# Kernel tuning notes

Measured on AMD Instinct MI355X. Metric: run time of the kernel, lower is better.

The kernel has to match this reference:

```python
import jax, jax.numpy as jnp
import numpy as np

EPS = 1e-5


def setup_inputs() -> dict:
    key = jax.random.key(0)
    k1, k2, k3 = jax.random.split(key, 3)
    B, D, T = 16, 256, 4096
    K = 2048
    x = jax.random.normal(k1, (B, D, T), dtype=jnp.float32)
    embedding_sum = jax.random.normal(k2, (K, D), dtype=jnp.float32)
    cluster_usage = jax.random.uniform(k3, (K,), dtype=jnp.float32)
    return {"x": x, "embedding_sum": embedding_sum, "cluster_usage": cluster_usage}


def reference(x, embedding_sum, cluster_usage):
    # embedding property: embedding_sum / clamp(cluster_usage, min=eps)
    emb = embedding_sum / jnp.clip(cluster_usage, EPS, None)[:, None]  # [K, D]
    B, D, T = x.shape
    x_flat = jnp.transpose(x, (0, 2, 1)).reshape(B * T, D)  # (b t) d
    # compute faithfully (clamped for numerical safety).
    x2 = jnp.sum(x_flat * x_flat, axis=-1, keepdims=True)      # [BT, 1]
    e2 = jnp.sum(emb * emb, axis=-1)                           # [K]
    d2 = x2 - 2.0 * (x_flat @ emb.T) + e2[None, :]             # [BT, K]
    distances = jnp.sqrt(jnp.clip(d2, 0.0, None))
    codes = jnp.argmin(distances, axis=-1).reshape(B, 1, T)    # int codes
    # decode: embedding gather, b t d -> b d t
    decoded = jnp.transpose(emb[codes[:, 0, :]], (0, 2, 1))    # [B, D, T]
    return codes, decoded
```

## Files before the change

kernel.cpp:

```cpp
#include <hip/hip_runtime.h>
#include <hip/hip_fp16.h>
#include <cmath>

#define EPS 1e-5f
#define TAU 0.15f
#define RP  8

#define Bn 16
#define Dn 256
#define Tn 4096
#define Kn 2048

typedef unsigned short ushort_t;
typedef __attribute__((ext_vector_type(8))) _Float16 f16x8;
typedef __attribute__((ext_vector_type(4))) float f32x4;

__device__ __forceinline__ unsigned short f2h(float v) {
    return __half_as_ushort(__float2half_rn(v));
}

#define GLOAD_LDS16(gp, lp) __builtin_amdgcn_global_load_lds( \
    (const __attribute__((address_space(1))) unsigned int*)(gp), \
    (__attribute__((address_space(3))) unsigned int*)(lp), 16, 0, 0)

__global__ __launch_bounds__(256) void prep_kernel(
    const float* __restrict__ es, const float* __restrict__ usage,
    float* __restrict__ emb, ushort_t* __restrict__ e16,
    float* __restrict__ bias, float4* __restrict__ embT4,
    int* __restrict__ counter)
{
    __shared__ float sh[256];
    __shared__ float wsum[4];
    const int k = blockIdx.x;
    const int d = threadIdx.x;
    const float inv = 1.0f / fmaxf(usage[k], EPS);
    const float v = es[(size_t)k * Dn + d] * inv;
    emb[(size_t)k * Dn + d] = v;
    e16[(size_t)k * Dn + d] = f2h(fminf(fmaxf(v, -65504.f), 65504.f));
    sh[d] = v;
    float sq = v * v;
    #pragma unroll
    for (int off = 32; off > 0; off >>= 1) sq += __shfl_down(sq, off, 64);
    const int lane = d & 63, wv = d >> 6;
    if (lane == 0) wsum[wv] = sq;
    __syncthreads();
    if (d < 64)
        embT4[(size_t)d * Kn + k] = make_float4(sh[4*d], sh[4*d+1], sh[4*d+2], sh[4*d+3]);
    if (d == 0) {
        bias[k] = 0.5f * (wsum[0] + wsum[1] + wsum[2] + wsum[3]);
        if (k == 0) *counter = 0;
    }
}

#define BARRIER_PIN()                                                         \
    __builtin_amdgcn_s_barrier();                                             \
    __builtin_amdgcn_sched_barrier(0)

#define STAGE_B(dst, kcc, hh)                                                 \
    {                                                                         \
        _Pragma("unroll")                                                     \
        for (int r = 0; r < 4; ++r) {                                         \
            const int c   = r * 512 + tid;                                    \
            const int row = c >> 4;                                           \
            const int col = (((c & 15) ^ (row & 15)) << 3);                   \
            GLOAD_LDS16(e16 + ((size_t)((kcc) * 128 + row)) * Dn + (hh) * 128 + col, \
                        (dst) + ((r * 512 + (wid << 6)) << 3));               \
        }                                                                     \
    }

#define COMPUTE_ACC(bbuf, afArr)                                              \
    {                                                                         \
        __builtin_amdgcn_s_setprio(1);                                        \
        _Pragma("unroll")                                                     \
        for (int ks = 0; ks < 4; ++ks)                                        \
            _Pragma("unroll")                                                 \
            for (int j = 0; j < 8; ++j) {                                     \
                const f16x8 bf = *(const f16x8*)(                             \
                    &(bbuf)[((j << 4) + l15) * 128 +                          \
                            ((((ks << 2) | quad) ^ l15) << 3)]);              \
                _Pragma("unroll")                                             \
                for (int i = 0; i < 2; ++i)                                   \
                    acc[i][j] = __builtin_amdgcn_mfma_f32_16x16x32_f16(       \
                        afArr[ks * 2 + i], bf, acc[i][j], 0, 0, 0);           \
            }                                                                 \
        __builtin_amdgcn_s_setprio(0);                                        \
    }

__global__ __launch_bounds__(512, 2) void gemm_argmax(
    const float* __restrict__ x, const ushort_t* __restrict__ e16,
    const float* __restrict__ bias_g, int* __restrict__ codes_i,
    float* __restrict__ codes_f, int* __restrict__ list,
    int* __restrict__ counter)
{
    __shared__ __align__(16) ushort_t BsS[2][128 * 128];
    __shared__ __align__(16) float    biasLds[2048];

    const int bid = blockIdx.x;
    const int b   = bid >> 4;
    const int tt  = bid & 15;
    const int t0  = tt << 8;

    const int tid  = threadIdx.x;
    const int lane = tid & 63;
    const int wid  = tid >> 6;
    const int l15  = lane & 15;
    const int quad = lane >> 4;
    const int wm   = wid;

    const size_t bTt0 = (size_t)b * Tn + t0;

    GLOAD_LDS16(bias_g + (tid << 2), biasLds + (wid << 8));

    f16x8 af0[8], af1[8];
    {
        const float* xb = x + (size_t)b * Dn * Tn;
        #pragma unroll
        for (int ks = 0; ks < 4; ++ks)
            #pragma unroll
            for (int i = 0; i < 2; ++i) {
                const int t = t0 + (wm << 5) + (i << 4) + l15;
                const float* c0 = xb + ((size_t)(ks * 32 + quad * 8)) * Tn + t;
                const float* c1 = c0 + (size_t)128 * Tn;
                f16x8 v0, v1;
                #pragma unroll
                for (int e = 0; e < 8; ++e) {
                    v0[e] = (_Float16)c0[(size_t)e * Tn];
                    v1[e] = (_Float16)c1[(size_t)e * Tn];
                }
                af0[ks * 2 + i] = v0;
                af1[ks * 2 + i] = v1;
            }
    }

    f32x4 acc[2][8];
    float S1[2][4], S2[2][4];
    int   K1[2][4];
    #pragma unroll
    for (int i = 0; i < 2; ++i)
        #pragma unroll
        for (int r = 0; r < 4; ++r) { S1[i][r] = -INFINITY; S2[i][r] = -INFINITY; K1[i][r] = 0; }
    #pragma unroll
    for (int i = 0; i < 2; ++i)
        #pragma unroll
        for (int j = 0; j < 8; ++j)
            acc[i][j] = (f32x4){-INFINITY, -INFINITY, -INFINITY, -INFINITY};

    asm volatile("s_waitcnt vmcnt(0)" ::: "memory");
    BARRIER_PIN();
    STAGE_B(&BsS[0][0], 0, 0);
    STAGE_B(&BsS[1][0], 0, 1);

    #pragma unroll 1
    for (int kc = 0; kc < 16; ++kc) {
        asm volatile("s_waitcnt vmcnt(4)" ::: "memory");
        BARRIER_PIN();
        {
            float bj[8];
            #pragma unroll
            for (int j = 0; j < 8; ++j)
                bj[j] = biasLds[(kc << 7) + (j << 4) + l15];
            const int kdrb = ((kc - 1) << 7) + l15;
            __builtin_amdgcn_s_setprio(1);
            #pragma unroll
            for (int j = 0; j < 8; ++j) {
                const f16x8 bf0 = *(const f16x8*)(
                    &BsS[0][((j << 4) + l15) * 128 + ((quad ^ l15) << 3)]);
                const float nb = -bj[j];
                const f32x4 cin = {nb, nb, nb, nb};
                const int kdr = kdrb + (j << 4);
                #pragma unroll
                for (int i = 0; i < 2; ++i) {
                    #pragma unroll
                    for (int r = 0; r < 4; ++r) {
                        const float s = acc[i][j][r];
                        S2[i][r] = __builtin_amdgcn_fmed3f(s, S1[i][r], S2[i][r]);
                        const bool gt = s > S1[i][r];
                        K1[i][r] = gt ? kdr : K1[i][r];
                        S1[i][r] = fmaxf(S1[i][r], s);
                    }
                    acc[i][j] = __builtin_amdgcn_mfma_f32_16x16x32_f16(
                        af0[i], bf0, cin, 0, 0, 0);
                }
            }
            #pragma unroll
            for (int ks = 1; ks < 4; ++ks)
                #pragma unroll
                for (int j = 0; j < 8; ++j) {
                    const f16x8 bf = *(const f16x8*)(
                        &BsS[0][((j << 4) + l15) * 128 +
                                ((((ks << 2) | quad) ^ l15) << 3)]);
                    #pragma unroll
                    for (int i = 0; i < 2; ++i)
                        acc[i][j] = __builtin_amdgcn_mfma_f32_16x16x32_f16(
                            af0[ks * 2 + i], bf, acc[i][j], 0, 0, 0);
                }
            __builtin_amdgcn_s_setprio(0);
        }
        BARRIER_PIN();
        if (kc < 15) STAGE_B(&BsS[0][0], kc + 1, 0);

        if (kc < 15) { asm volatile("s_waitcnt vmcnt(4)" ::: "memory"); }
        else         { asm volatile("s_waitcnt vmcnt(0)" ::: "memory"); }
        BARRIER_PIN();
        COMPUTE_ACC((&BsS[1][0]), af1);
        BARRIER_PIN();
        if (kc < 15) STAGE_B(&BsS[1][0], kc + 1, 1);
    }

    __builtin_amdgcn_sched_barrier(0);

    {
        const int kfb = (15 << 7) + l15;
        #pragma unroll
        for (int j = 0; j < 8; ++j) {
            const int kf = kfb + (j << 4);
            #pragma unroll
            for (int i = 0; i < 2; ++i)
                #pragma unroll
                for (int r = 0; r < 4; ++r) {
                    const float s = acc[i][j][r];
                    S2[i][r] = __builtin_amdgcn_fmed3f(s, S1[i][r], S2[i][r]);
                    const bool gt = s > S1[i][r];
                    K1[i][r] = gt ? kf : K1[i][r];
                    S1[i][r] = fmaxf(S1[i][r], s);
                }
        }
    }

    #pragma unroll
    for (int m = 1; m <= 8; m <<= 1) {
        #pragma unroll
        for (int i = 0; i < 2; ++i)
            #pragma unroll
            for (int r = 0; r < 4; ++r) {
                const float os1 = __shfl_xor(S1[i][r], m);
                const float os2 = __shfl_xor(S2[i][r], m);
                const int   ok1 = __shfl_xor(K1[i][r], m);
                const bool take = (os1 > S1[i][r]) || (os1 == S1[i][r] && ok1 < K1[i][r]);
                const float ns2 = take ? fmaxf(S1[i][r], os2) : fmaxf(S2[i][r], os1);
                if (take) { S1[i][r] = os1; K1[i][r] = ok1; }
                S2[i][r] = ns2;
            }
    }

    if (l15 == 0) {
        #pragma unroll
        for (int i = 0; i < 2; ++i)
            #pragma unroll
            for (int r = 0; r < 4; ++r) {
                const int row = (wm << 5) + (i << 4) + (quad << 2) + r;
                const size_t p = bTt0 + row;
                const int wk = K1[i][r];
                codes_i[p] = wk;
                codes_f[p] = (float)wk;
                if (S1[i][r] - S2[i][r] < TAU) {
                    const int idx = atomicAdd(counter, 1);
                    list[idx] = (int)p;
                }
            }
    }
}

__global__ __launch_bounds__(256) void rescue_kernel(
    const float* __restrict__ x, const float4* __restrict__ embT4,
    const float* __restrict__ bias, const int* __restrict__ list,
    const int* __restrict__ counter, int* __restrict__ codes_i,
    float* __restrict__ codes_f)
{
    __shared__ float xv[RP][256];
    __shared__ int plist[RP];
    __shared__ float rs[RP][4];
    __shared__ int   rk[RP][4];
    const int tid = threadIdx.x, lane = tid & 63, wid = tid >> 6;
    const int count = *counter;
    for (int base = blockIdx.x * RP; base < count; base += gridDim.x * RP) {
        const int npts = min(RP, count - base);
        __syncthreads();
        if (tid < npts) plist[tid] = list[base + tid];
        __syncthreads();
        for (int pi = 0; pi < npts; ++pi) {
            const int p = plist[pi];
            xv[pi][tid] = x[((size_t)((p >> 12) * Dn + tid)) * Tn + (p & 4095)];
        }
        for (int pi = npts; pi < RP; ++pi) xv[pi][tid] = 0.f;
        __syncthreads();

        float acc[8][RP];
        #pragma unroll
        for (int s = 0; s < 8; ++s)
            #pragma unroll
            for (int pi = 0; pi < RP; ++pi) acc[s][pi] = 0.f;

        for (int dc = 0; dc < 64; ++dc) {
            float4 ev[8];
            #pragma unroll
            for (int s = 0; s < 8; ++s)
                ev[s] = embT4[(size_t)dc * Kn + tid + (s << 8)];
            #pragma unroll
            for (int pi = 0; pi < RP; ++pi) {
                const float4 xw = *(const float4*)&xv[pi][dc << 2];
                #pragma unroll
                for (int s = 0; s < 8; ++s)
                    acc[s][pi] += ev[s].x * xw.x + ev[s].y * xw.y
                                + ev[s].z * xw.z + ev[s].w * xw.w;
            }
        }

        float bs[RP]; int bk[RP];
        #pragma unroll
        for (int pi = 0; pi < RP; ++pi) { bs[pi] = -INFINITY; bk[pi] = 0; }
        #pragma unroll
        for (int s = 0; s < 8; ++s) {
            const int kk = tid + (s << 8);
            const float bv = bias[kk];
            #pragma unroll
            for (int pi = 0; pi < RP; ++pi) {
                const float sc = acc[s][pi] - bv;
                if (sc > bs[pi]) { bs[pi] = sc; bk[pi] = kk; }
            }
        }
        #pragma unroll
        for (int off = 1; off < 64; off <<= 1) {
            #pragma unroll
            for (int pi = 0; pi < RP; ++pi) {
                const float os = __shfl_xor(bs[pi], off);
                const int   ok = __shfl_xor(bk[pi], off);
                if (os > bs[pi] || (os == bs[pi] && ok < bk[pi])) { bs[pi] = os; bk[pi] = ok; }
            }
        }
        if (lane == 0) {
            #pragma unroll
            for (int pi = 0; pi < RP; ++pi) { rs[pi][wid] = bs[pi]; rk[pi][wid] = bk[pi]; }
        }
        __syncthreads();
        if (tid < npts) {
            float fs = rs[tid][0]; int fk = rk[tid][0];
            #pragma unroll
            for (int w = 1; w < 4; ++w) {
                if (rs[tid][w] > fs || (rs[tid][w] == fs && rk[tid][w] < fk)) {
                    fs = rs[tid][w]; fk = rk[tid][w];
                }
            }
            const int p = plist[tid];
            codes_i[p] = fk;
            codes_f[p] = (float)fk;
        }
    }
}

__global__ __launch_bounds__(256) void decode_kernel(
    const float* __restrict__ emb, const int* __restrict__ codes,
    float* __restrict__ out)
{
    const int b = blockIdx.y;
    const int t = blockIdx.x * 256 + threadIdx.x;
    const int z16 = blockIdx.z * 16;
    const int c = codes[(size_t)b * Tn + t];
    const float4* e4 = (const float4*)(emb + (size_t)c * Dn);
    float* ob = out + (size_t)b * Dn * Tn + t;
    #pragma unroll 4
    for (int q = 0; q < 16; ++q) {
        const int d4 = z16 + q;
        const float4 v = e4[d4];
        ob[(size_t)(d4 * 4 + 0) * Tn] = v.x;
        ob[(size_t)(d4 * 4 + 1) * Tn] = v.y;
        ob[(size_t)(d4 * 4 + 2) * Tn] = v.z;
        ob[(size_t)(d4 * 4 + 3) * Tn] = v.w;
    }
}

extern "C" void kernel_launch(void* const* d_in, const int* in_sizes, int n_in,
                              void* d_out, int out_size, void* d_ws, size_t ws_size,
                              hipStream_t stream) {
    const float* x     = (const float*)d_in[0];
    const float* es    = (const float*)d_in[1];
    const float* usage = (const float*)d_in[2];

    char* ws = (char*)d_ws;
    float*    emb     = (float*)(ws + 0);
    float*    bias    = (float*)(ws + 2097152);
    ushort_t* e16     = (ushort_t*)(ws + 2105344);
    float4*   embT4   = (float4*)(ws + 3153920);
    int*      codes_i = (int*)(ws + 5251072);
    int*      list    = (int*)(ws + 5513216);
    int*      counter = (int*)(ws + 5775360);

    float* codes_f = (float*)d_out;
    float* decoded = (float*)d_out + (size_t)Bn * Tn;

    prep_kernel<<<Kn, 256, 0, stream>>>(es, usage, emb, e16, bias, embT4, counter);

    gemm_argmax<<<256, 512, 0, stream>>>(x, e16, bias, codes_i, codes_f,
                                         list, counter);

    rescue_kernel<<<1024, 256, 0, stream>>>(x, embT4, bias, list, counter, codes_i, codes_f);

    dim3 g6(Tn / 256, Bn, 4);
    decode_kernel<<<g6, 256, 0, stream>>>(emb, codes_i, decoded);
}
```

Before: 309.9 us.

## Split codebook across two blocks per tile and merge top-2 results

The GEMM-argmax grid is doubled so each output tile is handled by two blocks, each scanning half the codebook. Each block writes its best score, a rounded-up fp16 second-best and its index into a scratch record stored in the decoded output buffer. A new merge kernel combines the two halves, writes the codes and appends ambiguous points to the rescue list. This is meant to raise occupancy across the GPU's CUs (256 blocks at 2 per CU underfills the device), at the cost of an extra launch and extra global traffic for the records.

```diff
diff --git a/kernel.cpp b/kernel.cpp
--- a/kernel.cpp
+++ b/kernel.cpp
@@ -17,6 +17,14 @@
 
 __device__ __forceinline__ unsigned short f2h(float v) {
     return __half_as_ushort(__float2half_rn(v));
+}
+
+__device__ __forceinline__ unsigned short f16_up(float v) {
+    const __half h = __float2half_rn(v);
+    const float back = __half2float(h);
+    unsigned short u = __half_as_ushort(h);
+    if (back < v) u = (u & 0x8000u) ? (u - 1) : (u + 1);
+    return u;
 }
 
 #define GLOAD_LDS16(gp, lp) __builtin_amdgcn_global_load_lds( \
@@ -56,14 +64,14 @@
     __builtin_amdgcn_s_barrier();                                             \
     __builtin_amdgcn_sched_barrier(0)
 
-#define STAGE_B(dst, kcc, hh)                                                 \
+#define STAGE_B(dst, gc, hh)                                                  \
     {                                                                         \
         _Pragma("unroll")                                                     \
         for (int r = 0; r < 4; ++r) {                                         \
             const int c   = r * 512 + tid;                                    \
             const int row = c >> 4;                                           \
             const int col = (((c & 15) ^ (row & 15)) << 3);                   \
-            GLOAD_LDS16(e16 + ((size_t)((kcc) * 128 + row)) * Dn + (hh) * 128 + col, \
+            GLOAD_LDS16(e16 + ((size_t)((gc) * 128 + row)) * Dn + (hh) * 128 + col, \
                         (dst) + ((r * 512 + (wid << 6)) << 3));               \
         }                                                                     \
     }
@@ -88,17 +96,18 @@
 
 __global__ __launch_bounds__(512, 2) void gemm_argmax(
     const float* __restrict__ x, const ushort_t* __restrict__ e16,
-    const float* __restrict__ bias_g, int* __restrict__ codes_i,
-    float* __restrict__ codes_f, int* __restrict__ list,
-    int* __restrict__ counter)
+    const float* __restrict__ bias_g, uint2* __restrict__ rec)
 {
     __shared__ __align__(16) ushort_t BsS[2][128 * 128];
     __shared__ __align__(16) float    biasLds[2048];
 
-    const int bid = blockIdx.x;
-    const int b   = bid >> 4;
-    const int tt  = bid & 15;
-    const int t0  = tt << 8;
+    const int bid  = blockIdx.x;
+    const int kh   = bid >> 8;
+    const int tile = bid & 255;
+    const int b    = tile >> 4;
+    const int tt   = tile & 15;
+    const int t0   = tt << 8;
+    const int kc0  = kh << 3;
 
     const int tid  = threadIdx.x;
     const int lane = tid & 63;
@@ -147,19 +156,21 @@
 
     asm volatile("s_waitcnt vmcnt(0)" ::: "memory");
     BARRIER_PIN();
-    STAGE_B(&BsS[0][0], 0, 0);
-    STAGE_B(&BsS[1][0], 0, 1);
+    STAGE_B(&BsS[0][0], kc0, 0);
+    STAGE_B(&BsS[1][0], kc0, 1);
 
     #pragma unroll 1
-    for (int kc = 0; kc < 16; ++kc) {
+    for (int kc = 0; kc < 8; ++kc) {
+        const int g = kc0 + kc;
+
         asm volatile("s_waitcnt vmcnt(4)" ::: "memory");
         BARRIER_PIN();
         {
             float bj[8];
             #pragma unroll
             for (int j = 0; j < 8; ++j)
-                bj[j] = biasLds[(kc << 7) + (j << 4) + l15];
-            const int kdrb = ((kc - 1) << 7) + l15;
+                bj[j] = biasLds[(g << 7) + (j << 4) + l15];
+            const int kdrb = ((g - 1) << 7) + l15;
             __builtin_amdgcn_s_setprio(1);
             #pragma unroll
             for (int j = 0; j < 8; ++j) {
@@ -197,20 +208,20 @@
             __builtin_amdgcn_s_setprio(0);
         }
         BARRIER_PIN();
-        if (kc < 15) STAGE_B(&BsS[0][0], kc + 1, 0);
-
-        if (kc < 15) { asm volatile("s_waitcnt vmcnt(4)" ::: "memory"); }
-        else         { asm volatile("s_waitcnt vmcnt(0)" ::: "memory"); }
+        if (kc < 7) STAGE_B(&BsS[0][0], g + 1, 0);
+
+        if (kc < 7) { asm volatile("s_waitcnt vmcnt(4)" ::: "memory"); }
+        else        { asm volatile("s_waitcnt vmcnt(0)" ::: "memory"); }
         BARRIER_PIN();
         COMPUTE_ACC((&BsS[1][0]), af1);
         BARRIER_PIN();
-        if (kc < 15) STAGE_B(&BsS[1][0], kc + 1, 1);
+        if (kc < 7) STAGE_B(&BsS[1][0], g + 1, 1);
     }
 
     __builtin_amdgcn_sched_barrier(0);
 
     {
-        const int kfb = (15 << 7) + l15;
+        const int kfb = ((kc0 + 7) << 7) + l15;
         #pragma unroll
         for (int j = 0; j < 8; ++j) {
             const int kf = kfb + (j << 4);
@@ -250,14 +261,38 @@
             for (int r = 0; r < 4; ++r) {
                 const int row = (wm << 5) + (i << 4) + (quad << 2) + r;
                 const size_t p = bTt0 + row;
-                const int wk = K1[i][r];
-                codes_i[p] = wk;
-                codes_f[p] = (float)wk;
-                if (S1[i][r] - S2[i][r] < TAU) {
-                    const int idx = atomicAdd(counter, 1);
-                    list[idx] = (int)p;
-                }
-            }
+                uint2 e;
+                e.x = __float_as_uint(S1[i][r]);
+                e.y = ((unsigned)f16_up(S2[i][r]) << 16) | (unsigned)K1[i][r];
+                rec[(size_t)kh * (Bn * Tn) + p] = e;
+            }
+    }
+}
+
+__global__ __launch_bounds__(256) void merge_kernel(
+    const uint2* __restrict__ rec, int* __restrict__ codes_i,
+    float* __restrict__ codes_f, int* __restrict__ list, int* __restrict__ counter)
+{
+    const int p = blockIdx.x * 256 + threadIdx.x;
+    uint2 e = rec[p];
+    float g1 = __uint_as_float(e.x);
+    float g2 = __half2float(__ushort_as_half((unsigned short)(e.y >> 16)));
+    int kk = (int)(e.y & 0xffffu);
+    e = rec[(size_t)(Bn * Tn) + p];
+    const float s1 = __uint_as_float(e.x);
+    if (s1 > g1) {
+        const float s2u = __half2float(__ushort_as_half((unsigned short)(e.y >> 16)));
+        g2 = fmaxf(fmaxf(g2, g1), s2u);
+        g1 = s1;
+        kk = (int)(e.y & 0xffffu);
+    } else {
+        g2 = fmaxf(g2, s1);
+    }
+    codes_i[p] = kk;
+    codes_f[p] = (float)kk;
+    if (g1 - g2 < TAU) {
+        const int idx = atomicAdd(counter, 1);
+        list[idx] = p;
     }
 }
 
@@ -388,10 +423,14 @@
     float* codes_f = (float*)d_out;
     float* decoded = (float*)d_out + (size_t)Bn * Tn;
 
+    uint2* rec = (uint2*)decoded;
+
     prep_kernel<<<Kn, 256, 0, stream>>>(es, usage, emb, e16, bias, embT4, counter);
 
-    gemm_argmax<<<256, 512, 0, stream>>>(x, e16, bias, codes_i, codes_f,
-                                         list, counter);
+    gemm_argmax<<<512, 512, 0, stream>>>(x, e16, bias, rec);
+
+    merge_kernel<<<(Bn * Tn) / 256, 256, 0, stream>>>(rec, codes_i, codes_f,
+                                                      list, counter);
 
     rescue_kernel<<<1024, 256, 0, stream>>>(x, embT4, bias, list, counter, codes_i, codes_f);
 
```

Measured after the change: 339.1 us. 1.09x slower.
